# Performance work log

Measured on AMD Instinct MI355X. Metric: run time of the kernel, lower is better.

Reference implementation:

```python
import jax, jax.numpy as jnp
import numpy as np

B, LC, LP, D, H = 16, 1024, 1024, 128, 4
PFEAT = 1024  # hardcoded p_param rows in the original module


def _xavier(k, shape, gain=1.414):
    fan_in, fan_out = shape[-2], shape[-1]
    a = gain * np.sqrt(6.0 / (fan_in + fan_out))
    return jax.random.uniform(k, shape, minval=-a, maxval=a, dtype=jnp.float32)


def setup_inputs() -> dict:
    key = jax.random.key(0)
    ks = jax.random.split(key, 24)
    inp = {
        "c": jax.random.normal(ks[0], (B, LC, 1), dtype=jnp.float32),
        "c_mask": jnp.ones((B, LC), dtype=jnp.float32),
        "p": jax.random.normal(ks[1], (B, LP, PFEAT), dtype=jnp.float32),
        "p_mask": jnp.ones((B, LP), dtype=jnp.float32),
        # learned params; linear weights stored as [in, out] (transposed vs torch)
        "c_param": _xavier(ks[2], (1, D)),
        "p_param": _xavier(ks[3], (PFEAT, D)),
        "U": _xavier(ks[4], (H, D, D)),
        "W_p2c": _xavier(ks[5], (H, D, D)),
        "b_p2c": jnp.zeros((H, D), dtype=jnp.float32),
        "W_c2p": _xavier(ks[6], (H, D, D)),
        "b_c2p": jnp.zeros((H, D), dtype=jnp.float32),
        "Wh_c": _xavier(ks[7], (H, D, D)),
        "bh_c": jnp.zeros((H, D), dtype=jnp.float32),
        "Wh_p": _xavier(ks[8], (H, D, D)),
        "bh_p": jnp.zeros((H, D), dtype=jnp.float32),
        "Wa_c": _xavier(ks[9], (H, 2 * D, 1))[..., 0],  # [H, 2D]
        "ba_c": jnp.zeros((H,), dtype=jnp.float32),
        "Wa_p": _xavier(ks[10], (H, 2 * D, 1))[..., 0],
        "ba_p": jnp.zeros((H,), dtype=jnp.float32),
        "W_comb_c": _xavier(ks[11], (H * D, D)),
        "b_comb_c": jnp.zeros((D,), dtype=jnp.float32),
        "W_comb_p": _xavier(ks[12], (H * D, D)),
        "b_comb_p": jnp.zeros((D,), dtype=jnp.float32),
    }
    return inp


def _mask_softmax(a, mask):
    # a, mask broadcastable; softmax over last axis with mask applied post-exp
    a_max = jnp.max(a, axis=-1, keepdims=True)
    e = jnp.exp(a - a_max) * mask
    return e / (jnp.sum(e, axis=-1, keepdims=True) + 1e-6)


def reference(c, c_mask, p, p_mask, c_param, p_param, U, W_p2c, b_p2c,
              W_c2p, b_c2p, Wh_c, bh_c, Wh_p, bh_p, Wa_c, ba_c, Wa_p, ba_p,
              W_comb_c, b_comb_c, W_comb_p, b_comb_p):
    b = c.shape[0]
    cv = jnp.matmul(c, c_param)          # [b, Lc, d]
    pv = jnp.matmul(p, p_param)          # [b, Lp, d]

    # bilinear attention map per head: [b, H, Lc, Lp]
    A = jnp.tanh(jnp.einsum("bld,hde,bme->bhlm", cv, U, pv))
    A = A * (c_mask[:, None, :, None] * p_mask[:, None, None, :])

    pt = jnp.tanh(jnp.einsum("bmd,hde->bhme", pv, W_p2c) + b_p2c[None, :, None, :])
    c_trans = jnp.einsum("bhlm,bhme->bhle", A, pt)      # [b,H,Lc,d]
    ct = jnp.tanh(jnp.einsum("bld,hde->bhle", cv, W_c2p) + b_c2p[None, :, None, :])
    p_trans = jnp.einsum("bhlm,bhle->bhme", A, ct)      # [b,H,Lp,d]

    hc = jnp.tanh(jnp.einsum("bld,hde->bhle", cv, Wh_c) + bh_c[None, :, None, :])
    hp = jnp.tanh(jnp.einsum("bmd,hde->bhme", pv, Wh_p) + bh_p[None, :, None, :])

    # attention logits: linear over concat([hidden, trans]) -> split the weight
    score_c = (jnp.einsum("bhle,he->bhl", hc, Wa_c[:, :128])
               + jnp.einsum("bhle,he->bhl", c_trans, Wa_c[:, 128:])
               + ba_c[None, :, None])
    score_p = (jnp.einsum("bhme,he->bhm", hp, Wa_p[:, :128])
               + jnp.einsum("bhme,he->bhm", p_trans, Wa_p[:, 128:])
               + ba_p[None, :, None])

    c_att = _mask_softmax(score_c, c_mask[:, None, :])  # [b,H,Lc]
    p_att = _mask_softmax(score_p, p_mask[:, None, :])  # [b,H,Lp]

    cf = jnp.einsum("bld,bhl->bhd", cv, c_att).reshape(b, -1)  # [b, H*d]
    pf = jnp.einsum("bmd,bhm->bhd", pv, p_att).reshape(b, -1)

    cf_final = cf @ W_comb_c + b_comb_c  # [b, d]
    pf_final = pf @ W_comb_p + b_comb_p  # [b, d]
    return cf_final[:, :, None] * pf_final[:, None, :]  # [b, d, d]
```

## Files before the change

### kernel.cpp

```cpp
#include <hip/hip_runtime.h>


using bf16x8 = __attribute__((ext_vector_type(8))) short;
using u16x8  = __attribute__((ext_vector_type(8))) unsigned short;
using f32x4  = __attribute__((ext_vector_type(4))) float;

#define TWO_LOG2E 2.8853900817779268f

__device__ __forceinline__ float exp2_raw(float x){
#if __has_builtin(__builtin_amdgcn_exp2f)
  return __builtin_amdgcn_exp2f(x);
#else
  float r; asm("v_exp_f32 %0, %1" : "=v"(r) : "v"(x)); return r;
#endif
}
__device__ __forceinline__ float tanh_fast(float x){
  float e = exp2_raw(x * TWO_LOG2E);
  return fmaf(-2.0f, __builtin_amdgcn_rcpf(e + 1.0f), 1.0f);
}
__device__ __forceinline__ unsigned short f2bf(float f){
  unsigned u = __float_as_uint(f);
  u = (u + 0x7FFFu + ((u >> 16) & 1u)) >> 16;
  return (unsigned short)u;
}
__device__ __forceinline__ float bf2f(unsigned short s){
  return __uint_as_float((unsigned)s << 16);
}
__device__ __forceinline__ unsigned cvt_pk_bf16(float a, float b){
  unsigned r;
  asm("v_cvt_pk_bf16_f32 %0, %1, %2" : "=v"(r) : "v"(a), "v"(b));
  return r;
}
__device__ __forceinline__ void split8(const float4& x, const float4& y, bf16x8& hi, bf16x8& lo){
  unsigned h0 = cvt_pk_bf16(x.x, x.y);
  unsigned h1 = cvt_pk_bf16(x.z, x.w);
  unsigned h2 = cvt_pk_bf16(y.x, y.y);
  unsigned h3 = cvt_pk_bf16(y.z, y.w);
  float r0 = x.x - __uint_as_float(h0 << 16);
  float r1 = x.y - __uint_as_float(h0 & 0xffff0000u);
  float r2 = x.z - __uint_as_float(h1 << 16);
  float r3 = x.w - __uint_as_float(h1 & 0xffff0000u);
  float r4 = y.x - __uint_as_float(h2 << 16);
  float r5 = y.y - __uint_as_float(h2 & 0xffff0000u);
  float r6 = y.z - __uint_as_float(h3 << 16);
  float r7 = y.w - __uint_as_float(h3 & 0xffff0000u);
  uint4 H = make_uint4(h0, h1, h2, h3);
  uint4 L = make_uint4(cvt_pk_bf16(r0, r1), cvt_pk_bf16(r2, r3),
                       cvt_pk_bf16(r4, r5), cvt_pk_bf16(r6, r7));
  hi = __builtin_bit_cast(bf16x8, H);
  lo = __builtin_bit_cast(bf16x8, L);
}

__global__ __launch_bounds__(256) void ka_prep(
    const float* __restrict__ c_param,
    const float* __restrict__ U, const float* __restrict__ W_comb_c,
    const float* __restrict__ Wh_c, const float* __restrict__ W_c2p,
    const float* __restrict__ p_param, const float* __restrict__ W_p2c,
    const float* __restrict__ Wh_p,
    float* __restrict__ uh, float* __restrict__ wccv,
    float* __restrict__ whc_v, float* __restrict__ wc2p_v,
    unsigned short* __restrict__ ppT_hi, unsigned short* __restrict__ ppT_lo,
    unsigned short* __restrict__ wp2cT_hi, unsigned short* __restrict__ wp2cT_lo,
    unsigned short* __restrict__ whpT_hi, unsigned short* __restrict__ whpT_lo)
{
  __shared__ float T[64*68];
  int bid0 = blockIdx.x, t = threadIdx.x;
  if (bid0 < 4) {
    int h = bid0;
    if (t < 128) {
      float s_uh = 0.f, s_wcc = 0.f, s_whc = 0.f, s_wc2p = 0.f;
      for (int d = 0; d < 128; ++d) {
        float cp = c_param[d];
        s_uh   += cp * U[(h*128 + d)*128 + t];
        s_wcc  += cp * W_comb_c[(h*128 + d)*128 + t];
        s_whc  += cp * Wh_c[(h*128 + d)*128 + t];
        s_wc2p += cp * W_c2p[(h*128 + d)*128 + t];
      }
      uh[h*128 + t]     = s_uh;
      wccv[h*128 + t]   = s_wcc;
      whc_v[h*128 + t]  = s_whc;
      wc2p_v[h*128 + t] = s_wc2p;
    }
    return;
  }
  int bid = bid0 - 4;
  const float* src; unsigned short* dh; unsigned short* dl;
  int k0, e0, dpitch, drow0;
  if (bid < 32) {
    k0 = (bid >> 1)*64; e0 = (bid & 1)*64;
    src = p_param; dh = ppT_hi; dl = ppT_lo; dpitch = 1024; drow0 = e0;
  } else if (bid < 48) {
    int w = bid - 32; int h = w >> 2, ki = (w >> 1) & 1, ej = w & 1;
    k0 = ki*64; e0 = ej*64;
    src = W_p2c + h*16384; dh = wp2cT_hi; dl = wp2cT_lo; dpitch = 128;
    drow0 = h*128 + e0;
  } else {
    int w = bid - 48; int h = w >> 2, ki = (w >> 1) & 1, ej = w & 1;
    k0 = ki*64; e0 = ej*64;
    src = Wh_p + h*16384; dh = whpT_hi; dl = whpT_lo; dpitch = 128;
    drow0 = h*128 + e0;
  }
  {
    int r = t >> 2, cs = (t & 3)*4;
    const float* s = src + (k0 + r)*128 + e0 + cs;
    #pragma unroll
    for (int j = 0; j < 4; ++j) {
      float4 v = *(const float4*)(s + j*16);
      *(float4*)&T[r*68 + cs + j*16] = v;
    }
  }
  __syncthreads();
  {
    int e = t >> 2, ks = (t & 3)*16;
    unsigned short hs[16], ls[16];
    #pragma unroll
    for (int j = 0; j < 16; ++j) {
      float v = T[(ks + j)*68 + e];
      unsigned short hh = f2bf(v);
      hs[j] = hh; ls[j] = f2bf(v - bf2f(hh));
    }
    unsigned short* ph = dh + (drow0 + e)*dpitch + k0 + ks;
    unsigned short* pl = dl + (drow0 + e)*dpitch + k0 + ks;
    *(u16x8*)ph       = *(u16x8*)&hs[0];
    *(u16x8*)(ph + 8) = *(u16x8*)&hs[8];
    *(u16x8*)pl       = *(u16x8*)&ls[0];
    *(u16x8*)(pl + 8) = *(u16x8*)&ls[8];
  }
}

__global__ __launch_bounds__(256) void kb_pv_maps(
    const float* __restrict__ p,
    const unsigned short* __restrict__ ppT_hi, const unsigned short* __restrict__ ppT_lo,
    float* __restrict__ pv_part0, float* __restrict__ pv_part1,
    const float* __restrict__ c, const float* __restrict__ c_mask,
    const float* __restrict__ whc_v, const float* __restrict__ wc2p_v,
    const float* __restrict__ bh_c, const float* __restrict__ b_c2p,
    const float* __restrict__ Wa_c, const float* __restrict__ Wa_p,
    const float* __restrict__ ba_c,
    float* __restrict__ score_c, float2* __restrict__ pairP)
{
  __shared__ __align__(16) char smem[36864];
  int bid = blockIdx.x, t = threadIdx.x;
  if (bid < 512) {
    short* Bh = (short*)smem;
    short* Bl = (short*)(smem + 18432);
    int khalf = bid >> 8, rowtile = bid & 255;
    int kbase = khalf * 512;
    int row0 = rowtile * 64;
    float* __restrict__ pvp = khalf ? pv_part1 : pv_part0;
    int w = t >> 6, lane = t & 63;
    int l15 = lane & 15, l4 = lane >> 4;

    int bcol = t >> 1, bkh = (t & 1) * 32;
    const unsigned short* gBh = ppT_hi + bcol*1024 + kbase + bkh;
    const unsigned short* gBl = ppT_lo + bcol*1024 + kbase + bkh;
    short* sBh = &Bh[bcol*72 + bkh];
    short* sBl = &Bl[bcol*72 + bkh];

    const float* gA = p + (row0 + w*16 + l15)*1024 + kbase + l4*8;

    u16x8 rb[8];
    float4 ra[4];

    #pragma unroll
    for (int j = 0; j < 4; ++j) {
      rb[j]   = *(const u16x8*)(gBh + j*8);
      rb[4+j] = *(const u16x8*)(gBl + j*8);
    }
    #pragma unroll
    for (int j = 0; j < 4; ++j)
      ra[j] = *(const float4*)(gA + (j>>1)*32 + (j&1)*4);

    f32x4 acc[8];
    #pragma unroll
    for (int n = 0; n < 8; ++n) acc[n] = (f32x4){0.f,0.f,0.f,0.f};

    for (int kc = 0; kc < 8; ++kc) {
      __syncthreads();
      #pragma unroll
      for (int j = 0; j < 4; ++j) {
        *(u16x8*)(sBh + j*8) = rb[j];
        *(u16x8*)(sBl + j*8) = rb[4+j];
      }
      if (kc < 7) {
        #pragma unroll
        for (int j = 0; j < 4; ++j) {
          rb[j]   = *(const u16x8*)(gBh + (kc+1)*64 + j*8);
          rb[4+j] = *(const u16x8*)(gBl + (kc+1)*64 + j*8);
        }
      }
      float4 ran0, ran1, ran2, ran3;
      if (kc < 7) {
        const float* gAn = gA + (kc+1)*64;
        ran0 = *(const float4*)(gAn);
        ran1 = *(const float4*)(gAn + 4);
        ran2 = *(const float4*)(gAn + 32);
        ran3 = *(const float4*)(gAn + 36);
      }
      __syncthreads();
      #pragma unroll
      for (int ks = 0; ks < 2; ++ks) {
        bf16x8 ah, al;
        split8(ra[2*ks], ra[2*ks+1], ah, al);
        #pragma unroll
        for (int ct = 0; ct < 8; ++ct) {
          bf16x8 bh = *(const bf16x8*)&Bh[(ct*16 + l15)*72 + ks*32 + l4*8];
          bf16x8 bl = *(const bf16x8*)&Bl[(ct*16 + l15)*72 + ks*32 + l4*8];
          acc[ct] = __builtin_amdgcn_mfma_f32_16x16x32_bf16(ah, bh, acc[ct], 0, 0, 0);
          acc[ct] = __builtin_amdgcn_mfma_f32_16x16x32_bf16(ah, bl, acc[ct], 0, 0, 0);
          acc[ct] = __builtin_amdgcn_mfma_f32_16x16x32_bf16(al, bh, acc[ct], 0, 0, 0);
        }
      }
      if (kc < 7) { ra[0] = ran0; ra[1] = ran1; ra[2] = ran2; ra[3] = ran3; }
    }

    #pragma unroll
    for (int ct = 0; ct < 8; ++ct) {
      int col = ct*16 + l15;
      #pragma unroll
      for (int r = 0; r < 4; ++r) {
        int row = row0 + w*16 + l4*4 + r;
        pvp[row*128 + col] = acc[ct][r];
      }
    }
  } else {
    float* fsh = (float*)smem;
    float* whc_l  = fsh;
    float* wc2p_l = fsh + 128;
    float* bhc_l  = fsh + 256;
    float* bc2p_l = fsh + 384;
    float* wac1_l = fsh + 512;
    float* wap2_l = fsh + 640;
    int i = bid - 512;
    int b = i >> 4, h = (i >> 2) & 3, lc = i & 3;
    if (t < 128) {
      whc_l[t]  = whc_v[h*128 + t];
      wc2p_l[t] = wc2p_v[h*128 + t];
      bhc_l[t]  = bh_c[h*128 + t];
      bc2p_l[t] = b_c2p[h*128 + t];
      wac1_l[t] = Wa_c[h*256 + t];
      wap2_l[t] = Wa_p[h*256 + 128 + t];
    }
    __syncthreads();
    int l = lc*256 + t;
    float cl = c[b*1024 + l];
    float a1 = 0.f, a2 = 0.f;
    #pragma unroll 4
    for (int e = 0; e < 128; ++e) {
      a1 += wac1_l[e] * tanh_fast(cl*whc_l[e]  + bhc_l[e]);
      a2 += wap2_l[e] * tanh_fast(cl*wc2p_l[e] + bc2p_l[e]);
    }
    int o = (b*4 + h)*1024 + l;
    score_c[o] = a1 + ba_c[h];
    pairP[o] = make_float2(TWO_LOG2E * cl, c_mask[b*1024 + l] * a2);
  }
}

__global__ __launch_bounds__(256) void kc_head(
    const float* __restrict__ pv0, const float* __restrict__ pv1,
    const unsigned short* __restrict__ wp2cT_hi, const unsigned short* __restrict__ wp2cT_lo,
    const unsigned short* __restrict__ whpT_hi, const unsigned short* __restrict__ whpT_lo,
    const float* __restrict__ b_p2c, const float* __restrict__ bh_p,
    const float* __restrict__ Wa_c, const float* __restrict__ Wa_p,
    const float* __restrict__ p_mask, const float* __restrict__ ba_p,
    const float* __restrict__ uh,
    float2* __restrict__ pairC, float* __restrict__ score_p,
    float* __restrict__ g_arr, float* __restrict__ pv_sum)
{
  __shared__ __align__(16) short Whs[64*136];
  __shared__ __align__(16) short Wls[64*136];
  int t = threadIdx.x;
  int bid = blockIdx.x;
  int ph = bid >> 8, mtile = bid & 255;
  int path = ph >> 2, h = ph & 3;
  int w = t >> 6, lane = t & 63;
  int l15 = lane & 15, l4 = lane >> 4;

  const unsigned short* Wgh = (path ? whpT_hi : wp2cT_hi) + h*16384;
  const unsigned short* Wgl = (path ? whpT_lo : wp2cT_lo) + h*16384;
  int e2 = t >> 2, k0s = (t & 3)*32;

  u16x8 wr_h[4], wr_l[4];
  {
    const u16x8* sh = (const u16x8*)(Wgh + e2*128 + k0s);
    const u16x8* sl = (const u16x8*)(Wgl + e2*128 + k0s);
    #pragma unroll
    for (int j = 0; j < 4; ++j) { wr_h[j] = sh[j]; wr_l[j] = sl[j]; }
  }

  const float* bias_g = path ? bh_p : b_p2c;
  float biasv[8], wav[8];
  #pragma unroll
  for (int n = 0; n < 8; ++n) {
    int col = n*16 + l15;
    biasv[n] = bias_g[h*128 + col];
    wav[n]   = path ? Wa_p[h*256 + col] : Wa_c[h*256 + 128 + col];
  }

  int rowbase = mtile*64 + w*16;
  bf16x8 afh[4], afl[4];
  float gacc = 0.f;
  {
    int off = (rowbase + l15)*128 + l4*8;
    #pragma unroll
    for (int kt = 0; kt < 4; ++kt) {
      float4 x0 = *(const float4*)(pv0 + off + kt*32);
      float4 y0 = *(const float4*)(pv0 + off + kt*32 + 4);
      float4 x1 = *(const float4*)(pv1 + off + kt*32);
      float4 y1 = *(const float4*)(pv1 + off + kt*32 + 4);
      float4 x = make_float4(x0.x+x1.x, x0.y+x1.y, x0.z+x1.z, x0.w+x1.w);
      float4 y = make_float4(y0.x+y1.x, y0.y+y1.y, y0.z+y1.z, y0.w+y1.w);
      if (ph == 0) {
        *(float4*)(pv_sum + off + kt*32)     = x;
        *(float4*)(pv_sum + off + kt*32 + 4) = y;
      }
      split8(x, y, afh[kt], afl[kt]);
      if (!path) {
        float4 u0 = *(const float4*)(uh + h*128 + kt*32 + l4*8);
        float4 u1 = *(const float4*)(uh + h*128 + kt*32 + l4*8 + 4);
        gacc += x.x*u0.x + x.y*u0.y + x.z*u0.z + x.w*u0.w
              + y.x*u1.x + y.y*u1.y + y.z*u1.z + y.w*u1.w;
      }
    }
  }
  if (!path) {
    float gg = gacc;
    gg += __shfl_xor(gg, 16, 64);
    gg += __shfl_xor(gg, 32, 64);
    if (l4 == 0) {
      int grow = rowbase + l15;
      int bb = grow >> 10, m = grow & 1023;
      int idx = (bb*4 + h)*1024 + m;
      g_arr[idx] = gg;
      pairC[idx].x = TWO_LOG2E * gg;
    }
  }

  f32x4 acc[8];
  #pragma unroll
  for (int n = 0; n < 8; ++n) acc[n] = (f32x4){0.f,0.f,0.f,0.f};

  {
    u16x8* dhh = (u16x8*)&Whs[e2*136 + k0s];
    u16x8* dll = (u16x8*)&Wls[e2*136 + k0s];
    #pragma unroll
    for (int j = 0; j < 4; ++j) { dhh[j] = wr_h[j]; dll[j] = wr_l[j]; }
  }
  __syncthreads();
  {
    const u16x8* sh = (const u16x8*)(Wgh + (64 + e2)*128 + k0s);
    const u16x8* sl = (const u16x8*)(Wgl + (64 + e2)*128 + k0s);
    #pragma unroll
    for (int j = 0; j < 4; ++j) { wr_h[j] = sh[j]; wr_l[j] = sl[j]; }
  }
  #pragma unroll
  for (int n = 0; n < 4; ++n) {
    #pragma unroll
    for (int kt = 0; kt < 4; ++kt) {
      bf16x8 bh = *(const bf16x8*)&Whs[(n*16 + l15)*136 + kt*32 + l4*8];
      bf16x8 bl = *(const bf16x8*)&Wls[(n*16 + l15)*136 + kt*32 + l4*8];
      acc[n] = __builtin_amdgcn_mfma_f32_16x16x32_bf16(afh[kt], bh, acc[n], 0, 0, 0);
      acc[n] = __builtin_amdgcn_mfma_f32_16x16x32_bf16(afh[kt], bl, acc[n], 0, 0, 0);
      acc[n] = __builtin_amdgcn_mfma_f32_16x16x32_bf16(afl[kt], bh, acc[n], 0, 0, 0);
    }
  }
  __syncthreads();
  {
    u16x8* dhh = (u16x8*)&Whs[e2*136 + k0s];
    u16x8* dll = (u16x8*)&Wls[e2*136 + k0s];
    #pragma unroll
    for (int j = 0; j < 4; ++j) { dhh[j] = wr_h[j]; dll[j] = wr_l[j]; }
  }
  __syncthreads();
  #pragma unroll
  for (int n = 0; n < 4; ++n) {
    int nn = 4 + n;
    #pragma unroll
    for (int kt = 0; kt < 4; ++kt) {
      bf16x8 bh = *(const bf16x8*)&Whs[(n*16 + l15)*136 + kt*32 + l4*8];
      bf16x8 bl = *(const bf16x8*)&Wls[(n*16 + l15)*136 + kt*32 + l4*8];
      acc[nn] = __builtin_amdgcn_mfma_f32_16x16x32_bf16(afh[kt], bh, acc[nn], 0, 0, 0);
      acc[nn] = __builtin_amdgcn_mfma_f32_16x16x32_bf16(afh[kt], bl, acc[nn], 0, 0, 0);
      acc[nn] = __builtin_amdgcn_mfma_f32_16x16x32_bf16(afl[kt], bh, acc[nn], 0, 0, 0);
    }
  }

  {
    float pp0 = 0.f, pp1 = 0.f, pp2 = 0.f, pp3 = 0.f;
    #pragma unroll
    for (int n = 0; n < 8; ++n) {
      float bb = biasv[n], ww = wav[n];
      pp0 += ww * tanh_fast(acc[n][0] + bb);
      pp1 += ww * tanh_fast(acc[n][1] + bb);
      pp2 += ww * tanh_fast(acc[n][2] + bb);
      pp3 += ww * tanh_fast(acc[n][3] + bb);
    }
    #pragma unroll
    for (int off = 1; off < 16; off <<= 1) {
      pp0 += __shfl_xor(pp0, off, 64);
      pp1 += __shfl_xor(pp1, off, 64);
      pp2 += __shfl_xor(pp2, off, 64);
      pp3 += __shfl_xor(pp3, off, 64);
    }
    if (l15 == 0) {
      int grow = rowbase + l4*4;
      int bb = grow >> 10, m = grow & 1023;
      int idx = (bb*4 + h)*1024 + m;
      if (path) {
        float bap = ba_p[h];
        *(float4*)&score_p[idx] = make_float4(pp0+bap, pp1+bap, pp2+bap, pp3+bap);
      } else {
        float4 mk = *(const float4*)&p_mask[bb*1024 + m];
        pairC[idx+0].y = mk.x * pp0;
        pairC[idx+1].y = mk.y * pp1;
        pairC[idx+2].y = mk.z * pp2;
        pairC[idx+3].y = mk.w * pp3;
      }
    }
  }
}

__global__ __launch_bounds__(256) void kd_scores(
    const float* __restrict__ c_mask, const float* __restrict__ p_mask,
    const float* __restrict__ g_arr,
    const float2* __restrict__ pairC, const float2* __restrict__ pairP,
    float* __restrict__ score_c, float* __restrict__ score_p)
{
  __shared__ float T[128*65];
  __shared__ float gm_s[64], ptw_s[64], pm_s[64];
  __shared__ float kl_s[128], ctw_s[128], cm_s[128];
  __shared__ float red[256];
  int bid = blockIdx.x, t = threadIdx.x;
  int bh = bid >> 7, tile = bid & 127;
  int b = bh >> 2;
  int l0 = (tile >> 4) * 128, m0 = (tile & 15) * 64;
  if (t < 64) {
    gm_s[t]  = g_arr[bh*1024 + m0 + t];
    ptw_s[t] = pairC[bh*1024 + m0 + t].y;
    pm_s[t]  = p_mask[b*1024 + m0 + t];
  } else if (t < 192) {
    int l = t - 64;
    float2 pp = pairP[bh*1024 + l0 + l];
    kl_s[l] = pp.x; ctw_s[l] = pp.y;
    cm_s[l] = c_mask[b*1024 + l0 + l];
  }
  __syncthreads();
  {
    int r = t >> 1, hm = t & 1;
    float kl = kl_s[r];
    float accc = 0.f;
    #pragma unroll 8
    for (int j = 0; j < 32; ++j) {
      int m = hm*32 + j;
      float e = exp2_raw(kl * gm_s[m]);
      float tt = fmaf(-2.0f, __builtin_amdgcn_rcpf(e + 1.0f), 1.0f);
      T[r*65 + m] = tt;
      accc = fmaf(ptw_s[m], tt, accc);
    }
    accc += __shfl_xor(accc, 1, 64);
    if (hm == 0) atomicAdd(score_c + bh*1024 + l0 + r, cm_s[r]*accc);
  }
  __syncthreads();
  {
    int col = t & 63, seg = t >> 6;
    float accp = 0.f;
    #pragma unroll 8
    for (int j = 0; j < 32; ++j) {
      int l = seg*32 + j;
      accp = fmaf(ctw_s[l], T[l*65 + col], accp);
    }
    red[t] = accp;
    __syncthreads();
    if (t < 64) {
      float total = red[t] + red[t+64] + red[t+128] + red[t+192];
      atomicAdd(score_p + bh*1024 + m0 + t, pm_s[t]*total);
    }
  }
}

__device__ __forceinline__ float blk_red_max(float v, float* red, int t){
  red[t] = v; __syncthreads();
  for (int s = 128; s; s >>= 1) { if (t < s) red[t] = fmaxf(red[t], red[t+s]); __syncthreads(); }
  float r = red[0]; __syncthreads();
  return r;
}
__device__ __forceinline__ float blk_red_sum(float v, float* red, int t){
  red[t] = v; __syncthreads();
  for (int s = 128; s; s >>= 1) { if (t < s) red[t] += red[t+s]; __syncthreads(); }
  float r = red[0]; __syncthreads();
  return r;
}

__global__ __launch_bounds__(256) void ke_soft(
    const float* __restrict__ c, const float* __restrict__ c_mask, const float* __restrict__ p_mask,
    const float* __restrict__ score_c, const float* __restrict__ score_p,
    const float* __restrict__ pv_sum,
    float* __restrict__ s_c, float* __restrict__ pf_part)
{
  __shared__ float sv[1024];
  __shared__ float red[256];
  int bid = blockIdx.x, t = threadIdx.x;
  if (bid < 64) {
    int b = bid >> 2, h = bid & 3, bh = b*4 + h;
    const float* sc = score_c + bh*1024;
    const float* mk = c_mask + b*1024;
    float v[4];
    float mx = -1e30f;
    #pragma unroll
    for (int j = 0; j < 4; ++j) { v[j] = sc[t + j*256]; mx = fmaxf(mx, v[j]); }
    mx = blk_red_max(mx, red, t);
    float sum = 0.f;
    #pragma unroll
    for (int j = 0; j < 4; ++j) {
      float e = exp2_raw((v[j] - mx) * 1.4426950408889634f) * mk[t + j*256];
      sv[t + j*256] = e;
      sum += e;
    }
    sum = blk_red_sum(sum, red, t);
    float rinv = __fdividef(1.0f, sum + 1e-6f);
    float a = 0.f;
    #pragma unroll
    for (int j = 0; j < 4; ++j) a += sv[t + j*256] * rinv * c[b*1024 + t + j*256];
    a = blk_red_sum(a, red, t);
    if (t == 0) s_c[bh] = a;
  } else {
    int i = bid - 64;
    int b = i >> 4, h = (i >> 2) & 3, ch = i & 3, bh = b*4 + h;
    const float* sc = score_p + bh*1024;
    const float* mk = p_mask + b*1024;
    float v[4];
    float mx = -1e30f;
    #pragma unroll
    for (int j = 0; j < 4; ++j) { v[j] = sc[t + j*256]; mx = fmaxf(mx, v[j]); }
    mx = blk_red_max(mx, red, t);
    float sum = 0.f;
    #pragma unroll
    for (int j = 0; j < 4; ++j) {
      float e = exp2_raw((v[j] - mx) * 1.4426950408889634f) * mk[t + j*256];
      sv[t + j*256] = e;
      sum += e;
    }
    sum = blk_red_sum(sum, red, t);
    float rinv = __fdividef(1.0f, sum + 1e-6f);
    int e0 = t & 127, seg = t >> 7;
    int mbase = ch*256 + seg*128;
    float acc = 0.f;
    const float* base = pv_sum + (b*1024 + mbase)*128 + e0;
    #pragma unroll 4
    for (int m = 0; m < 128; ++m) acc = fmaf(sv[mbase + m]*rinv, base[m*128], acc);
    red[t] = acc; __syncthreads();
    if (t < 128) pf_part[(ch*16 + b)*512 + h*128 + t] = red[t] + red[t + 128];
  }
}

__global__ __launch_bounds__(256) void kf_final(
    const float* __restrict__ s_c, const float* __restrict__ wccv,
    const float* __restrict__ b_comb_c, const float* __restrict__ pf_part,
    const float* __restrict__ W_comb_p, const float* __restrict__ b_comb_p,
    float* __restrict__ out)
{
  __shared__ float pfr[512];
  __shared__ float cfl[128], pfl[128];
  int b = blockIdx.x, t = threadIdx.x;
  #pragma unroll
  for (int s = 0; s < 2; ++s) {
    int idx = t + s*256;
    pfr[idx] = pf_part[(0*16 + b)*512 + idx] + pf_part[(1*16 + b)*512 + idx]
             + pf_part[(2*16 + b)*512 + idx] + pf_part[(3*16 + b)*512 + idx];
  }
  __syncthreads();
  if (t < 128) {
    float cf = b_comb_c[t];
    #pragma unroll
    for (int h = 0; h < 4; ++h) cf += s_c[b*4 + h] * wccv[h*128 + t];
    float pf = b_comb_p[t];
    #pragma unroll 8
    for (int i = 0; i < 512; ++i) pf += pfr[i] * W_comb_p[i*128 + t];
    cfl[t] = cf; pfl[t] = pf;
  }
  __syncthreads();
  #pragma unroll
  for (int k = 0; k < 64; ++k) {
    int idx = k*256 + t;
    out[b*16384 + idx] = cfl[idx >> 7] * pfl[idx & 127];
  }
}

extern "C" void kernel_launch(void* const* d_in, const int* in_sizes, int n_in,
                              void* d_out, int out_size, void* d_ws, size_t ws_size,
                              hipStream_t stream)
{
  const float* c        = (const float*)d_in[0];
  const float* c_mask   = (const float*)d_in[1];
  const float* p        = (const float*)d_in[2];
  const float* p_mask   = (const float*)d_in[3];
  const float* c_param  = (const float*)d_in[4];
  const float* p_param  = (const float*)d_in[5];
  const float* U        = (const float*)d_in[6];
  const float* W_p2c    = (const float*)d_in[7];
  const float* b_p2c    = (const float*)d_in[8];
  const float* W_c2p    = (const float*)d_in[9];
  const float* b_c2p    = (const float*)d_in[10];
  const float* Wh_c     = (const float*)d_in[11];
  const float* bh_c     = (const float*)d_in[12];
  const float* Wh_p     = (const float*)d_in[13];
  const float* bh_p     = (const float*)d_in[14];
  const float* Wa_c     = (const float*)d_in[15];
  const float* ba_c     = (const float*)d_in[16];
  const float* Wa_p     = (const float*)d_in[17];
  const float* ba_p     = (const float*)d_in[18];
  const float* W_comb_c = (const float*)d_in[19];
  const float* b_comb_c = (const float*)d_in[20];
  const float* W_comb_p = (const float*)d_in[21];
  const float* b_comb_p = (const float*)d_in[22];
  float* out = (float*)d_out;

  char* ws = (char*)d_ws;
  float*          pv_part0 = (float*)         (ws + 0);
  float*          pv_part1 = (float*)         (ws + 8388608);
  float*          pv_sum   = (float*)         (ws + 16777216);
  unsigned short* ppT_hi   = (unsigned short*)(ws + 25165824);
  unsigned short* ppT_lo   = (unsigned short*)(ws + 25427968);
  unsigned short* wp2cT_hi = (unsigned short*)(ws + 25690112);
  unsigned short* wp2cT_lo = (unsigned short*)(ws + 25821184);
  unsigned short* whpT_hi  = (unsigned short*)(ws + 25952256);
  unsigned short* whpT_lo  = (unsigned short*)(ws + 26083328);
  float*          uh       = (float*)         (ws + 26214400);
  float*          wccv     = (float*)         (ws + 26216448);
  float*          whc_v    = (float*)         (ws + 26218496);
  float*          wc2p_v   = (float*)         (ws + 26220544);
  float*          g_arr    = (float*)         (ws + 26222592);
  float2*         pairC    = (float2*)        (ws + 26484736);
  float2*         pairP    = (float2*)        (ws + 27009024);
  float*          score_c  = (float*)         (ws + 27533312);
  float*          score_p  = (float*)         (ws + 27795456);
  float*          s_c      = (float*)         (ws + 28057600);
  float*          pf_part  = (float*)         (ws + 28057856);

  ka_prep<<<dim3(68), dim3(256), 0, stream>>>(
      c_param, U, W_comb_c, Wh_c, W_c2p, p_param, W_p2c, Wh_p,
      uh, wccv, whc_v, wc2p_v,
      ppT_hi, ppT_lo, wp2cT_hi, wp2cT_lo, whpT_hi, whpT_lo);

  kb_pv_maps<<<dim3(768), dim3(256), 0, stream>>>(
      p, ppT_hi, ppT_lo, pv_part0, pv_part1,
      c, c_mask, whc_v, wc2p_v, bh_c, b_c2p, Wa_c, Wa_p, ba_c,
      score_c, pairP);

  kc_head<<<dim3(2048), dim3(256), 0, stream>>>(
      pv_part0, pv_part1, wp2cT_hi, wp2cT_lo, whpT_hi, whpT_lo,
      b_p2c, bh_p, Wa_c, Wa_p, p_mask, ba_p, uh, pairC, score_p, g_arr, pv_sum);

  kd_scores<<<dim3(8192), dim3(256), 0, stream>>>(
      c_mask, p_mask, g_arr, pairC, pairP, score_c, score_p);

  ke_soft<<<dim3(320), dim3(256), 0, stream>>>(
      c, c_mask, p_mask, score_c, score_p, pv_sum, s_c, pf_part);

  kf_final<<<dim3(16), dim3(256), 0, stream>>>(
      s_c, wccv, b_comb_c, pf_part, W_comb_p, b_comb_p, out);
}
```

Baseline: 121.6 us.

## Split pv GEMM K into four partials and pack tanh tile as bf16

The p×p_param GEMM now splits K into four quarters instead of two, launching 1024 GEMM blocks so more CUs are busy, and kc_head sums four partial buffers. This raises parallelism at the cost of twice the partial-sum traffic (32 MB written and read). Separately, kd_scores stores its shared-memory tanh tile as packed bf16 pairs instead of fp32, halving LDS footprint and stores but lowering the precision of the score_p accumulation. The c-path branch indexing and workspace offsets are shifted to match.

```diff
diff --git a/kernel.cpp b/kernel.cpp
--- a/kernel.cpp
+++ b/kernel.cpp
@@ -131,7 +131,7 @@
 __global__ __launch_bounds__(256) void kb_pv_maps(
     const float* __restrict__ p,
     const unsigned short* __restrict__ ppT_hi, const unsigned short* __restrict__ ppT_lo,
-    float* __restrict__ pv_part0, float* __restrict__ pv_part1,
+    float* __restrict__ pv_parts,
     const float* __restrict__ c, const float* __restrict__ c_mask,
     const float* __restrict__ whc_v, const float* __restrict__ wc2p_v,
     const float* __restrict__ bh_c, const float* __restrict__ b_c2p,
@@ -141,13 +141,13 @@
 {
   __shared__ __align__(16) char smem[36864];
   int bid = blockIdx.x, t = threadIdx.x;
-  if (bid < 512) {
+  if (bid < 1024) {
     short* Bh = (short*)smem;
     short* Bl = (short*)(smem + 18432);
-    int khalf = bid >> 8, rowtile = bid & 255;
-    int kbase = khalf * 512;
+    int kq = bid >> 8, rowtile = bid & 255;
+    int kbase = kq * 256;
     int row0 = rowtile * 64;
-    float* __restrict__ pvp = khalf ? pv_part1 : pv_part0;
+    float* __restrict__ pvp = pv_parts + kq*2097152;
     int w = t >> 6, lane = t & 63;
     int l15 = lane & 15, l4 = lane >> 4;
 
@@ -175,14 +175,14 @@
     #pragma unroll
     for (int n = 0; n < 8; ++n) acc[n] = (f32x4){0.f,0.f,0.f,0.f};
 
-    for (int kc = 0; kc < 8; ++kc) {
+    for (int kc = 0; kc < 4; ++kc) {
       __syncthreads();
       #pragma unroll
       for (int j = 0; j < 4; ++j) {
         *(u16x8*)(sBh + j*8) = rb[j];
         *(u16x8*)(sBl + j*8) = rb[4+j];
       }
-      if (kc < 7) {
+      if (kc < 3) {
         #pragma unroll
         for (int j = 0; j < 4; ++j) {
           rb[j]   = *(const u16x8*)(gBh + (kc+1)*64 + j*8);
@@ -190,7 +190,7 @@
         }
       }
       float4 ran0, ran1, ran2, ran3;
-      if (kc < 7) {
+      if (kc < 3) {
         const float* gAn = gA + (kc+1)*64;
         ran0 = *(const float4*)(gAn);
         ran1 = *(const float4*)(gAn + 4);
@@ -211,7 +211,7 @@
           acc[ct] = __builtin_amdgcn_mfma_f32_16x16x32_bf16(al, bh, acc[ct], 0, 0, 0);
         }
       }
-      if (kc < 7) { ra[0] = ran0; ra[1] = ran1; ra[2] = ran2; ra[3] = ran3; }
+      if (kc < 3) { ra[0] = ran0; ra[1] = ran1; ra[2] = ran2; ra[3] = ran3; }
     }
 
     #pragma unroll
@@ -231,7 +231,7 @@
     float* bc2p_l = fsh + 384;
     float* wac1_l = fsh + 512;
     float* wap2_l = fsh + 640;
-    int i = bid - 512;
+    int i = bid - 1024;
     int b = i >> 4, h = (i >> 2) & 3, lc = i & 3;
     if (t < 128) {
       whc_l[t]  = whc_v[h*128 + t];
@@ -257,7 +257,7 @@
 }
 
 __global__ __launch_bounds__(256) void kc_head(
-    const float* __restrict__ pv0, const float* __restrict__ pv1,
+    const float* __restrict__ pv_parts,
     const unsigned short* __restrict__ wp2cT_hi, const unsigned short* __restrict__ wp2cT_lo,
     const unsigned short* __restrict__ whpT_hi, const unsigned short* __restrict__ whpT_lo,
     const float* __restrict__ b_p2c, const float* __restrict__ bh_p,
@@ -304,15 +304,22 @@
     int off = (rowbase + l15)*128 + l4*8;
     #pragma unroll
     for (int kt = 0; kt < 4; ++kt) {
-      float4 x0 = *(const float4*)(pv0 + off + kt*32);
-      float4 y0 = *(const float4*)(pv0 + off + kt*32 + 4);
-      float4 x1 = *(const float4*)(pv1 + off + kt*32);
-      float4 y1 = *(const float4*)(pv1 + off + kt*32 + 4);
-      float4 x = make_float4(x0.x+x1.x, x0.y+x1.y, x0.z+x1.z, x0.w+x1.w);
-      float4 y = make_float4(y0.x+y1.x, y0.y+y1.y, y0.z+y1.z, y0.w+y1.w);
+      int o2 = off + kt*32;
+      float4 x0 = *(const float4*)(pv_parts + o2);
+      float4 y0 = *(const float4*)(pv_parts + o2 + 4);
+      float4 x1 = *(const float4*)(pv_parts + 2097152 + o2);
+      float4 y1 = *(const float4*)(pv_parts + 2097152 + o2 + 4);
+      float4 x2 = *(const float4*)(pv_parts + 4194304 + o2);
+      float4 y2 = *(const float4*)(pv_parts + 4194304 + o2 + 4);
+      float4 x3 = *(const float4*)(pv_parts + 6291456 + o2);
+      float4 y3 = *(const float4*)(pv_parts + 6291456 + o2 + 4);
+      float4 x = make_float4((x0.x+x1.x)+(x2.x+x3.x), (x0.y+x1.y)+(x2.y+x3.y),
+                             (x0.z+x1.z)+(x2.z+x3.z), (x0.w+x1.w)+(x2.w+x3.w));
+      float4 y = make_float4((y0.x+y1.x)+(y2.x+y3.x), (y0.y+y1.y)+(y2.y+y3.y),
+                             (y0.z+y1.z)+(y2.z+y3.z), (y0.w+y1.w)+(y2.w+y3.w));
       if (ph == 0) {
-        *(float4*)(pv_sum + off + kt*32)     = x;
-        *(float4*)(pv_sum + off + kt*32 + 4) = y;
+        *(float4*)(pv_sum + o2)     = x;
+        *(float4*)(pv_sum + o2 + 4) = y;
       }
       split8(x, y, afh[kt], afl[kt]);
       if (!path) {
@@ -426,7 +433,7 @@
     const float2* __restrict__ pairC, const float2* __restrict__ pairP,
     float* __restrict__ score_c, float* __restrict__ score_p)
 {
-  __shared__ float T[128*65];
+  __shared__ unsigned Tp[128*33];
   __shared__ float gm_s[64], ptw_s[64], pm_s[64];
   __shared__ float kl_s[128], ctw_s[128], cm_s[128];
   __shared__ float red[256];
@@ -449,13 +456,15 @@
     int r = t >> 1, hm = t & 1;
     float kl = kl_s[r];
     float accc = 0.f;
-    #pragma unroll 8
-    for (int j = 0; j < 32; ++j) {
+    #pragma unroll 4
+    for (int j = 0; j < 32; j += 2) {
       int m = hm*32 + j;
-      float e = exp2_raw(kl * gm_s[m]);
-      float tt = fmaf(-2.0f, __builtin_amdgcn_rcpf(e + 1.0f), 1.0f);
-      T[r*65 + m] = tt;
-      accc = fmaf(ptw_s[m], tt, accc);
+      float e0 = exp2_raw(kl * gm_s[m]);
+      float e1 = exp2_raw(kl * gm_s[m+1]);
+      float t0 = fmaf(-2.0f, __builtin_amdgcn_rcpf(e0 + 1.0f), 1.0f);
+      float t1 = fmaf(-2.0f, __builtin_amdgcn_rcpf(e1 + 1.0f), 1.0f);
+      Tp[r*33 + hm*16 + (j>>1)] = cvt_pk_bf16(t0, t1);
+      accc = fmaf(ptw_s[m], t0, fmaf(ptw_s[m+1], t1, accc));
     }
     accc += __shfl_xor(accc, 1, 64);
     if (hm == 0) atomicAdd(score_c + bh*1024 + l0 + r, cm_s[r]*accc);
@@ -463,11 +472,14 @@
   __syncthreads();
   {
     int col = t & 63, seg = t >> 6;
+    int ci = col >> 1, sel = col & 1;
     float accp = 0.f;
     #pragma unroll 8
     for (int j = 0; j < 32; ++j) {
       int l = seg*32 + j;
-      accp = fmaf(ctw_s[l], T[l*65 + col], accp);
+      unsigned pk = Tp[l*33 + ci];
+      float tv = __uint_as_float(sel ? (pk & 0xffff0000u) : (pk << 16));
+      accp = fmaf(ctw_s[l], tv, accp);
     }
     red[t] = accp;
     __syncthreads();
@@ -616,39 +628,38 @@
   float* out = (float*)d_out;
 
   char* ws = (char*)d_ws;
-  float*          pv_part0 = (float*)         (ws + 0);
-  float*          pv_part1 = (float*)         (ws + 8388608);
-  float*          pv_sum   = (float*)         (ws + 16777216);
-  unsigned short* ppT_hi   = (unsigned short*)(ws + 25165824);
-  unsigned short* ppT_lo   = (unsigned short*)(ws + 25427968);
-  unsigned short* wp2cT_hi = (unsigned short*)(ws + 25690112);
-  unsigned short* wp2cT_lo = (unsigned short*)(ws + 25821184);
-  unsigned short* whpT_hi  = (unsigned short*)(ws + 25952256);
-  unsigned short* whpT_lo  = (unsigned short*)(ws + 26083328);
-  float*          uh       = (float*)         (ws + 26214400);
-  float*          wccv     = (float*)         (ws + 26216448);
-  float*          whc_v    = (float*)         (ws + 26218496);
-  float*          wc2p_v   = (float*)         (ws + 26220544);
-  float*          g_arr    = (float*)         (ws + 26222592);
-  float2*         pairC    = (float2*)        (ws + 26484736);
-  float2*         pairP    = (float2*)        (ws + 27009024);
-  float*          score_c  = (float*)         (ws + 27533312);
-  float*          score_p  = (float*)         (ws + 27795456);
-  float*          s_c      = (float*)         (ws + 28057600);
-  float*          pf_part  = (float*)         (ws + 28057856);
+  float*          pv_parts = (float*)         (ws + 0);
+  float*          pv_sum   = (float*)         (ws + 33554432);
+  unsigned short* ppT_hi   = (unsigned short*)(ws + 41943040);
+  unsigned short* ppT_lo   = (unsigned short*)(ws + 42205184);
+  unsigned short* wp2cT_hi = (unsigned short*)(ws + 42467328);
+  unsigned short* wp2cT_lo = (unsigned short*)(ws + 42598400);
+  unsigned short* whpT_hi  = (unsigned short*)(ws + 42729472);
+  unsigned short* whpT_lo  = (unsigned short*)(ws + 42860544);
+  float*          uh       = (float*)         (ws + 42991616);
+  float*          wccv     = (float*)         (ws + 42993664);
+  float*          whc_v    = (float*)         (ws + 42995712);
+  float*          wc2p_v   = (float*)         (ws + 42997760);
+  float*          g_arr    = (float*)         (ws + 42999808);
+  float2*         pairC    = (float2*)        (ws + 43261952);
+  float2*         pairP    = (float2*)        (ws + 43786240);
+  float*          score_c  = (float*)         (ws + 44310528);
+  float*          score_p  = (float*)         (ws + 44572672);
+  float*          s_c      = (float*)         (ws + 44834816);
+  float*          pf_part  = (float*)         (ws + 44835072);
 
   ka_prep<<<dim3(68), dim3(256), 0, stream>>>(
       c_param, U, W_comb_c, Wh_c, W_c2p, p_param, W_p2c, Wh_p,
       uh, wccv, whc_v, wc2p_v,
       ppT_hi, ppT_lo, wp2cT_hi, wp2cT_lo, whpT_hi, whpT_lo);
 
-  kb_pv_maps<<<dim3(768), dim3(256), 0, stream>>>(
-      p, ppT_hi, ppT_lo, pv_part0, pv_part1,
+  kb_pv_maps<<<dim3(1280), dim3(256), 0, stream>>>(
+      p, ppT_hi, ppT_lo, pv_parts,
       c, c_mask, whc_v, wc2p_v, bh_c, b_c2p, Wa_c, Wa_p, ba_c,
       score_c, pairP);
 
   kc_head<<<dim3(2048), dim3(256), 0, stream>>>(
-      pv_part0, pv_part1, wp2cT_hi, wp2cT_lo, whpT_hi, whpT_lo,
+      pv_parts, wp2cT_hi, wp2cT_lo, whpT_hi, whpT_lo,
       b_p2c, bh_p, Wa_c, Wa_p, p_mask, ba_p, uh, pairC, score_p, g_arr, pv_sum);
 
   kd_scores<<<dim3(8192), dim3(256), 0, stream>>>(
```

New measurement: 141.6 us. 1.16x slower.
